# Optimization experiments

Measured on AMD Instinct MI355X. Metric: run time of the kernel, lower is better.

The kernel has to match this reference:

```python
import jax, jax.numpy as jnp
import numpy as np

# 5x5 neighborhood offsets as (dx, dy), row-major as in the original delta list
DELTA = [(dx, dy) for dy in (-2, -1, 0, 1, 2) for dx in (-2, -1, 0, 1, 2)]
BN_EPS = 1e-5


def _conv(x, w, padding):
    return jax.lax.conv_general_dilated(
        x, w, window_strides=(1, 1), padding=padding,
        dimension_numbers=('NCHW', 'OIHW', 'NCHW'))


def setup_inputs() -> dict:
    key = jax.random.key(0)
    ks = jax.random.split(key, 4)
    B, C, H, W = 128, 256, 24, 24
    source_feature = jax.random.normal(ks[0], (B, C, H, W), jnp.float32)
    detection_feature = jax.random.normal(ks[1], (B, C, H, W), jnp.float32)
    w1 = jax.random.normal(ks[2], (256, 512, 3, 3), jnp.float32) * 0.02
    b1 = jnp.zeros((256,), jnp.float32)
    bn_gamma = jnp.ones((256,), jnp.float32)
    bn_beta = jnp.zeros((256,), jnp.float32)
    bn_mean = jnp.zeros((256,), jnp.float32)
    bn_var = jnp.ones((256,), jnp.float32)
    w2 = jax.random.normal(ks[3], (25, 256, 1, 1), jnp.float32) * 0.05
    b2 = jnp.zeros((25,), jnp.float32)
    return dict(source_feature=source_feature, detection_feature=detection_feature,
                w1=w1, b1=b1, bn_gamma=bn_gamma, bn_beta=bn_beta,
                bn_mean=bn_mean, bn_var=bn_var, w2=w2, b2=b2)


def reference(source_feature, detection_feature, w1, b1, bn_gamma, bn_beta,
              bn_mean, bn_var, w2, b2):
    B, C, H, W = source_feature.shape
    # kernel_pre: Conv3x3(512->256, pad 1) + BN + ReLU + Conv1x1(256->25)
    concat_f = jnp.concatenate([source_feature, detection_feature], axis=1)  # [B,512,H,W]
    x = _conv(concat_f, w1, ((1, 1), (1, 1))) + b1[None, :, None, None]
    inv = bn_gamma / jnp.sqrt(bn_var + BN_EPS)
    x = x * inv[None, :, None, None] + (bn_beta - bn_mean * inv)[None, :, None, None]
    x = jax.nn.relu(x)
    logits = _conv(x, w2, ((0, 0), (0, 0))) + b2[None, :, None, None]  # [B,25,H,W]
    # per-pixel softmax over the 25 neighborhood taps
    kmaps = jax.nn.softmax(logits, axis=1)  # [B,25,H,W]
    # propagate: softmax-weighted 5x5 neighbor gather-sum; out-of-bounds taps
    # contribute zero (matches the skipped-boundary terms in the original loop)
    padded = jnp.pad(source_feature, ((0, 0), (0, 0), (2, 2), (2, 2)))
    prop = jnp.zeros_like(source_feature)
    for order, (dx, dy) in enumerate(DELTA):
        shifted = padded[:, :, 2 + dy:2 + dy + H, 2 + dx:2 + dx + W]  # [B,C,H,W]
        prop = prop + shifted * kmaps[:, order][:, None]  # broadcast over C
    return prop
```

## Files before the change

kernel.cpp:

```cpp
#include <hip/hip_runtime.h>
#include <hip/hip_bf16.h>
#include <stdint.h>

#define BATCH 128
#define CIN   256
#define CCAT  512
#define HH    24
#define WW    24
#define HP    26
#define WP    26
#define COUT  256
#define KDIM  4608
#define NPIX  576
#define MDIM  73728
#define NORD  25

typedef __attribute__((ext_vector_type(8))) short bf16x8;
typedef __attribute__((ext_vector_type(4))) float f32x4;

__device__ __forceinline__ unsigned short f2bf(float v) {
    union { float f; unsigned u; } x; x.f = v;
    unsigned r = x.u + 0x7fffu + ((x.u >> 16) & 1u);
    return (unsigned short)(r >> 16);
}
__device__ __forceinline__ float bf_lo(unsigned w) {
    union { unsigned u; float f; } x; x.u = w << 16; return x.f;
}
__device__ __forceinline__ float bf_hi(unsigned w) {
    union { unsigned u; float f; } x; x.u = w & 0xffff0000u; return x.f;
}

__device__ __forceinline__ void async_copy16(const void* gsrc, void* ldst) {
    __builtin_amdgcn_global_load_lds(
        (const __attribute__((address_space(1))) unsigned int*)gsrc,
        (__attribute__((address_space(3))) unsigned int*)ldst, 16, 0, 0);
}

#define PTILE 192
#define LSTR  72
__global__ __launch_bounds__(256) void prep_transpose(
        const float* __restrict__ src, const float* __restrict__ det,
        unsigned short* __restrict__ apad) {
    __shared__ unsigned short lds[PTILE * LSTR];
    int pt = blockIdx.x;
    int cg = blockIdx.y;
    int b  = blockIdx.z;
    int c0 = cg * 64;
    int p0 = pt * PTILE;
    const float* inp = (c0 < CIN)
        ? (src + ((long)b * CIN + c0) * NPIX)
        : (det + ((long)b * CIN + (c0 - CIN)) * NPIX);
    int tid = threadIdx.x;

    #pragma unroll
    for (int it = 0; it < 12; it++) {
        int l  = it * 256 + tid;
        int cq = l / PTILE;
        int px = l - cq * PTILE;
        const float* pb = inp + (long)cq * 4 * NPIX + p0 + px;
        unsigned short v0 = f2bf(pb[0 * NPIX]);
        unsigned short v1 = f2bf(pb[1 * NPIX]);
        unsigned short v2 = f2bf(pb[2 * NPIX]);
        unsigned short v3 = f2bf(pb[3 * NPIX]);
        uint2 w;
        w.x = (unsigned)v0 | ((unsigned)v1 << 16);
        w.y = (unsigned)v2 | ((unsigned)v3 << 16);
        *(uint2*)&lds[px * LSTR + cq * 4] = w;
    }
    __syncthreads();

    #pragma unroll
    for (int it = 0; it < 6; it++) {
        int l   = it * 256 + tid;
        int px  = l >> 3;
        int ch8 = l & 7;
        uint4 w = *(const uint4*)&lds[px * LSTR + ch8 * 8];
        int p  = p0 + px;
        int y  = p / WW, x = p - y * WW;
        long o = (((long)b * HP + (y + 1)) * WP + (x + 1)) * CCAT + c0 + ch8 * 8;
        *(uint4*)(apad + o) = w;
    }
}

__global__ __launch_bounds__(256) void zero_halo(unsigned short* __restrict__ apad) {
    int t = blockIdx.x * 256 + threadIdx.x;
    int ch8 = t & 63;
    int r   = t >> 6;
    int hp  = r % 100;
    int b   = r / 100;
    int y, x;
    if (hp < 26)      { y = 0;       x = hp; }
    else if (hp < 52) { y = 25;      x = hp - 26; }
    else if (hp < 76) { y = hp - 51; x = 0; }
    else              { y = hp - 75; x = 25; }
    long o = (((long)b * HP + y) * WP + x) * CCAT + ch8 * 8;
    *(uint4*)(apad + o) = (uint4){0u, 0u, 0u, 0u};
}

__global__ __launch_bounds__(256) void prep_w(
        const float* __restrict__ w1, const float* __restrict__ b1,
        const float* __restrict__ gam, const float* __restrict__ bet,
        const float* __restrict__ mu, const float* __restrict__ var,
        unsigned short* __restrict__ bt,
        float* __restrict__ scale, float* __restrict__ shift) {
    int idx = blockIdx.x * 256 + threadIdx.x;
    if (idx < COUT * KDIM) {
        int n = idx / KDIM;
        int k = idx - n * KDIM;
        int s = k >> 9;
        int ci = k & 511;
        int ky = s / 3, kx = s - ky * 3;
        float v = w1[(((long)n * 512 + ci) * 3 + ky) * 3 + kx];
        bt[idx] = f2bf(v);
    }
    if (blockIdx.x == 0 && threadIdx.x < COUT) {
        int c = threadIdx.x;
        float inv = gam[c] * rsqrtf(var[c] + 1e-5f);
        scale[c] = inv;
        shift[c] = (b1[c] - mu[c]) * inv + bet[c];
    }
}

#define STAGE_A(j, nb, soff) \
    async_copy16(apad + aSrc[j] + (soff), (void*)&lds[(nb)*32768 + (j)*4096 + w*512])
#define STAGE_B(j, nb, koff) \
    async_copy16(bt + bSrc[j] + (koff), (void*)&lds[(nb)*32768 + 16384 + (j)*4096 + w*512])
#define BAR()  __builtin_amdgcn_s_barrier()
#define WAITV2() { asm volatile("s_waitcnt vmcnt(2)" ::: "memory"); }
#define WAITV0() { asm volatile("s_waitcnt vmcnt(0)" ::: "memory"); }
#define WAITL()  { asm volatile("s_waitcnt lgkmcnt(0)" ::: "memory"); __builtin_amdgcn_sched_barrier(0); }

__global__ __launch_bounds__(512, 2) void conv1_gemm(
        const unsigned short* __restrict__ apad,
        const unsigned short* __restrict__ bt,
        const float* __restrict__ scale, const float* __restrict__ shift,
        unsigned short* __restrict__ xout) {
    __shared__ unsigned short lds[65536];
    const int tid  = threadIdx.x;
    const int w    = tid >> 6;
    const int lane = tid & 63;
    const int wr = w >> 2, wc = w & 3;
    const int fr = lane & 15, ls = lane >> 4;
    const long m0 = (long)blockIdx.x * 256;

    const int rowq = tid >> 3;
    const int sl   = (tid & 7) ^ (rowq & 7);
    long aSrc[4], bSrc[4];
    #pragma unroll
    for (int j = 0; j < 4; j++) {
        int r = j * 64 + rowq;
        long m = m0 + r;
        int b  = (int)(m / NPIX);
        int rr = (int)(m - (long)b * NPIX);
        int y = rr / WW, x = rr - y * WW;
        aSrc[j] = (((long)b * HP + y) * WP + x) * (long)CCAT + sl * 8;
        bSrc[j] = (long)r * KDIM + sl * 8;
    }

    const int rb   = fr & 7;
    const int csw0 = ((ls    ) ^ rb) << 4;
    const int csw1 = ((ls + 4) ^ rb) << 4;
    const int aBase = (wr * 128 + fr) * 128;
    const int bBase = 32768 + (wc * 64 + fr) * 128;

    f32x4 acc[8][4];
    #pragma unroll
    for (int i = 0; i < 8; i++)
        #pragma unroll
        for (int j = 0; j < 4; j++) acc[i][j] = (f32x4){0.f, 0.f, 0.f, 0.f};

    STAGE_B(0, 0, 0); STAGE_B(1, 0, 0); STAGE_B(2, 0, 0); STAGE_B(3, 0, 0);
    STAGE_A(0, 0, 0); STAGE_A(2, 0, 0); STAGE_A(1, 0, 0); STAGE_A(3, 0, 0);
    WAITV2();
    BAR();

    bf16x8 afr[4], bfr[4];
    int nb = 0;
    for (int kt = 0; kt < 71; kt++) {
        const int ktn = kt + 1;
        const int seg = ktn >> 3;
        const int ky = seg / 3, kx = seg - ky * 3;
        const long soff = (long)(ky * WP + kx) * CCAT + (ktn & 7) * 64;
        const long koff = (long)ktn * 64;
        const int pb = nb ^ 1;
        const char* L = (const char*)lds + nb * 65536;

        #pragma unroll
        for (int n = 0; n < 4; n++)
            bfr[n] = *(const bf16x8*)(L + bBase + n * 2048 + csw0);
        #pragma unroll
        for (int m = 0; m < 4; m++)
            afr[m] = *(const bf16x8*)(L + aBase + m * 2048 + csw0);
        STAGE_B(0, pb, koff); STAGE_B(1, pb, koff);
        WAITV2();
        BAR(); WAITL();
        __builtin_amdgcn_s_setprio(1);
        #pragma unroll
        for (int m = 0; m < 4; m++)
            #pragma unroll
            for (int n = 0; n < 4; n++)
                acc[m][n] = __builtin_amdgcn_mfma_f32_16x16x32_bf16(afr[m], bfr[n], acc[m][n], 0, 0, 0);
        __builtin_amdgcn_s_setprio(0);
        BAR();

        #pragma unroll
        for (int m = 0; m < 4; m++)
            afr[m] = *(const bf16x8*)(L + aBase + 8192 + m * 2048 + csw0);
        STAGE_B(2, pb, koff); STAGE_B(3, pb, koff);
        BAR(); WAITL();
        __builtin_amdgcn_s_setprio(1);
        #pragma unroll
        for (int m = 0; m < 4; m++)
            #pragma unroll
            for (int n = 0; n < 4; n++)
                acc[4 + m][n] = __builtin_amdgcn_mfma_f32_16x16x32_bf16(afr[m], bfr[n], acc[4 + m][n], 0, 0, 0);
        __builtin_amdgcn_s_setprio(0);
        BAR();

        #pragma unroll
        for (int n = 0; n < 4; n++)
            bfr[n] = *(const bf16x8*)(L + bBase + n * 2048 + csw1);
        #pragma unroll
        for (int m = 0; m < 4; m++)
            afr[m] = *(const bf16x8*)(L + aBase + m * 2048 + csw1);
        STAGE_A(0, pb, soff); STAGE_A(2, pb, soff);
        BAR(); WAITL();
        __builtin_amdgcn_s_setprio(1);
        #pragma unroll
        for (int m = 0; m < 4; m++)
            #pragma unroll
            for (int n = 0; n < 4; n++)
                acc[m][n] = __builtin_amdgcn_mfma_f32_16x16x32_bf16(afr[m], bfr[n], acc[m][n], 0, 0, 0);
        __builtin_amdgcn_s_setprio(0);
        BAR();

        #pragma unroll
        for (int m = 0; m < 4; m++)
            afr[m] = *(const bf16x8*)(L + aBase + 8192 + m * 2048 + csw1);
        STAGE_A(1, pb, soff); STAGE_A(3, pb, soff);
        WAITV2();
        BAR(); WAITL();
        __builtin_amdgcn_s_setprio(1);
        #pragma unroll
        for (int m = 0; m < 4; m++)
            #pragma unroll
            for (int n = 0; n < 4; n++)
                acc[4 + m][n] = __builtin_amdgcn_mfma_f32_16x16x32_bf16(afr[m], bfr[n], acc[4 + m][n], 0, 0, 0);
        __builtin_amdgcn_s_setprio(0);
        BAR();

        nb ^= 1;
    }

    {
        const char* L = (const char*)lds + nb * 65536;
        #pragma unroll
        for (int n = 0; n < 4; n++)
            bfr[n] = *(const bf16x8*)(L + bBase + n * 2048 + csw0);
        #pragma unroll
        for (int m = 0; m < 4; m++)
            afr[m] = *(const bf16x8*)(L + aBase + m * 2048 + csw0);
        WAITV0();
        BAR(); WAITL();
        #pragma unroll
        for (int m = 0; m < 4; m++)
            #pragma unroll
            for (int n = 0; n < 4; n++)
                acc[m][n] = __builtin_amdgcn_mfma_f32_16x16x32_bf16(afr[m], bfr[n], acc[m][n], 0, 0, 0);
        BAR();
        #pragma unroll
        for (int m = 0; m < 4; m++)
            afr[m] = *(const bf16x8*)(L + aBase + 8192 + m * 2048 + csw0);
        WAITL();
        #pragma unroll
        for (int m = 0; m < 4; m++)
            #pragma unroll
            for (int n = 0; n < 4; n++)
                acc[4 + m][n] = __builtin_amdgcn_mfma_f32_16x16x32_bf16(afr[m], bfr[n], acc[4 + m][n], 0, 0, 0);
        #pragma unroll
        for (int n = 0; n < 4; n++)
            bfr[n] = *(const bf16x8*)(L + bBase + n * 2048 + csw1);
        #pragma unroll
        for (int m = 0; m < 4; m++)
            afr[m] = *(const bf16x8*)(L + aBase + m * 2048 + csw1);
        WAITL();
        #pragma unroll
        for (int m = 0; m < 4; m++)
            #pragma unroll
            for (int n = 0; n < 4; n++)
                acc[m][n] = __builtin_amdgcn_mfma_f32_16x16x32_bf16(afr[m], bfr[n], acc[m][n], 0, 0, 0);
        #pragma unroll
        for (int m = 0; m < 4; m++)
            afr[m] = *(const bf16x8*)(L + aBase + 8192 + m * 2048 + csw1);
        WAITL();
        #pragma unroll
        for (int m = 0; m < 4; m++)
            #pragma unroll
            for (int n = 0; n < 4; n++)
                acc[4 + m][n] = __builtin_amdgcn_mfma_f32_16x16x32_bf16(afr[m], bfr[n], acc[4 + m][n], 0, 0, 0);
    }

    #pragma unroll
    for (int n = 0; n < 4; n++) {
        int col = wc * 64 + n * 16 + fr;
        float sc = scale[col], sh = shift[col];
        #pragma unroll
        for (int m = 0; m < 8; m++) {
            long rbase = m0 + wr * 128 + m * 16 + ls * 4;
            #pragma unroll
            for (int j = 0; j < 4; j++) {
                float v = acc[m][n][j] * sc + sh;
                v = v > 0.f ? v : 0.f;
                xout[(rbase + j) * COUT + col] = f2bf(v);
            }
        }
    }
}

__global__ __launch_bounds__(256) void conv2_softmax(
        const unsigned short* __restrict__ x, const float* __restrict__ w2,
        const float* __restrict__ b2, float* __restrict__ kmaps) {
    __shared__ float w2s[NORD * 256];
    __shared__ float b2s[NORD];
    for (int i = threadIdx.x; i < NORD * 256; i += 256) w2s[i] = w2[i];
    if (threadIdx.x < NORD) b2s[threadIdx.x] = b2[threadIdx.x];
    __syncthreads();
    long pix = (long)blockIdx.x * 256 + threadIdx.x;
    float acc[NORD];
    #pragma unroll
    for (int o = 0; o < NORD; o++) acc[o] = b2s[o];
    const unsigned short* xr = x + pix * COUT;
    for (int kc = 0; kc < 32; kc++) {
        uint4 raw = *(const uint4*)(xr + kc * 8);
        float xf[8];
        xf[0] = bf_lo(raw.x); xf[1] = bf_hi(raw.x);
        xf[2] = bf_lo(raw.y); xf[3] = bf_hi(raw.y);
        xf[4] = bf_lo(raw.z); xf[5] = bf_hi(raw.z);
        xf[6] = bf_lo(raw.w); xf[7] = bf_hi(raw.w);
        #pragma unroll
        for (int o = 0; o < NORD; o++) {
            const float* wrow = &w2s[o * 256 + kc * 8];
            float4 wa = *(const float4*)(wrow);
            float4 wb = *(const float4*)(wrow + 4);
            acc[o] += xf[0] * wa.x + xf[1] * wa.y + xf[2] * wa.z + xf[3] * wa.w
                    + xf[4] * wb.x + xf[5] * wb.y + xf[6] * wb.z + xf[7] * wb.w;
        }
    }
    float mx = acc[0];
    #pragma unroll
    for (int o = 1; o < NORD; o++) mx = fmaxf(mx, acc[o]);
    float s = 0.f;
    #pragma unroll
    for (int o = 0; o < NORD; o++) { acc[o] = expf(acc[o] - mx); s += acc[o]; }
    float inv = 1.f / s;
    float* kout = kmaps + pix * NORD;
    #pragma unroll
    for (int o = 0; o < NORD; o++) kout[o] = acc[o] * inv;
}

__global__ __launch_bounds__(576) void propagate(
        const float* __restrict__ src, const float* __restrict__ kmaps,
        float* __restrict__ out) {
    __shared__ float sm[28 * 28];
    int b  = blockIdx.y;
    int cg = blockIdx.x;
    int tid = threadIdx.x;
    int y = tid / 24, x = tid - y * 24;
    float km[NORD];
    const float* kp = kmaps + ((long)b * NPIX + tid) * NORD;
    #pragma unroll
    for (int o = 0; o < NORD; o++) km[o] = kp[o];
    for (int c = 0; c < 16; c++) {
        int cc = cg * 16 + c;
        const float* sp = src + ((long)b * CIN + cc) * NPIX;
        __syncthreads();
        for (int t = tid; t < 28 * 28; t += 576) {
            int yy = t / 28, xx = t - yy * 28;
            float v = 0.f;
            if (yy >= 2 && yy < 26 && xx >= 2 && xx < 26)
                v = sp[(yy - 2) * 24 + (xx - 2)];
            sm[t] = v;
        }
        __syncthreads();
        float a = 0.f;
        #pragma unroll
        for (int o = 0; o < NORD; o++) {
            int dy = o / 5 - 2, dx = o % 5 - 2;
            a += km[o] * sm[(y + 2 + dy) * 28 + (x + 2 + dx)];
        }
        out[((long)b * CIN + cc) * NPIX + tid] = a;
    }
}

extern "C" void kernel_launch(void* const* d_in, const int* in_sizes, int n_in,
                              void* d_out, int out_size, void* d_ws, size_t ws_size,
                              hipStream_t stream) {
    const float* src = (const float*)d_in[0];
    const float* det = (const float*)d_in[1];
    const float* w1  = (const float*)d_in[2];
    const float* b1  = (const float*)d_in[3];
    const float* gam = (const float*)d_in[4];
    const float* bet = (const float*)d_in[5];
    const float* mu  = (const float*)d_in[6];
    const float* var = (const float*)d_in[7];
    const float* w2  = (const float*)d_in[8];
    const float* b2  = (const float*)d_in[9];
    float* out = (float*)d_out;

    char* ws = (char*)d_ws;
    size_t off = 0;
    unsigned short* apad = (unsigned short*)(ws + off); off += (size_t)BATCH * HP * WP * CCAT * 2;
    unsigned short* bt   = (unsigned short*)(ws + off); off += (size_t)COUT * KDIM * 2;
    unsigned short* xbuf = (unsigned short*)(ws + off); off += (size_t)MDIM * COUT * 2;
    float* kmaps = (float*)(ws + off); off += (size_t)MDIM * NORD * 4;
    float* scale = (float*)(ws + off); off += 1024;
    float* shift = (float*)(ws + off); off += 1024;

    zero_halo<<<3200, 256, 0, stream>>>(apad);
    prep_transpose<<<dim3(3, 8, BATCH), 256, 0, stream>>>(src, det, apad);
    prep_w<<<4608, 256, 0, stream>>>(w1, b1, gam, bet, mu, var, bt, scale, shift);
    conv1_gemm<<<288, 512, 0, stream>>>(apad, bt, scale, shift, xbuf);
    conv2_softmax<<<288, 256, 0, stream>>>(xbuf, w2, b2, kmaps);
    propagate<<<dim3(16, BATCH), 576, 0, stream>>>(src, kmaps, out);
}
```

Before: 417.7 us.

## Shrink conv GEMM tile to 192x128 with grid remap and reordered staging

```diff
diff --git a/kernel.cpp b/kernel.cpp
--- a/kernel.cpp
+++ b/kernel.cpp
@@ -121,10 +121,12 @@
     }
 }
 
+#define ABUF_SH 12288
+#define BUF_SH  20480
 #define STAGE_A(j, nb, soff) \
-    async_copy16(apad + aSrc[j] + (soff), (void*)&lds[(nb)*32768 + (j)*4096 + w*512])
+    async_copy16(apad + aSrc[j] + (soff), (void*)&lds[(nb)*BUF_SH + (j)*4096 + w*512])
 #define STAGE_B(j, nb, koff) \
-    async_copy16(bt + bSrc[j] + (koff), (void*)&lds[(nb)*32768 + 16384 + (j)*4096 + w*512])
+    async_copy16(bt + bSrc[j] + (koff), (void*)&lds[(nb)*BUF_SH + ABUF_SH + (j)*4096 + w*512])
 #define BAR()  __builtin_amdgcn_s_barrier()
 #define WAITV2() { asm volatile("s_waitcnt vmcnt(2)" ::: "memory"); }
 #define WAITV0() { asm volatile("s_waitcnt vmcnt(0)" ::: "memory"); }
@@ -135,46 +137,50 @@
         const unsigned short* __restrict__ bt,
         const float* __restrict__ scale, const float* __restrict__ shift,
         unsigned short* __restrict__ xout) {
-    __shared__ unsigned short lds[65536];
+    __shared__ unsigned short lds[40960];
     const int tid  = threadIdx.x;
     const int w    = tid >> 6;
     const int lane = tid & 63;
     const int wr = w >> 2, wc = w & 3;
     const int fr = lane & 15, ls = lane >> 4;
-    const long m0 = (long)blockIdx.x * 256;
+
+    const int Lb = blockIdx.x;
+    const int logical = (Lb & 7) * 96 + (Lb >> 3);
+    const int n0 = (logical & 1) * 128;
+    const long m0 = (long)(logical >> 1) * 192;
 
     const int rowq = tid >> 3;
     const int sl   = (tid & 7) ^ (rowq & 7);
-    long aSrc[4], bSrc[4];
-    #pragma unroll
-    for (int j = 0; j < 4; j++) {
+    long aSrc[3], bSrc[2];
+    #pragma unroll
+    for (int j = 0; j < 3; j++) {
         int r = j * 64 + rowq;
         long m = m0 + r;
         int b  = (int)(m / NPIX);
         int rr = (int)(m - (long)b * NPIX);
         int y = rr / WW, x = rr - y * WW;
         aSrc[j] = (((long)b * HP + y) * WP + x) * (long)CCAT + sl * 8;
-        bSrc[j] = (long)r * KDIM + sl * 8;
-    }
+    }
+    #pragma unroll
+    for (int j = 0; j < 2; j++)
+        bSrc[j] = (long)(n0 + j * 64 + rowq) * KDIM + sl * 8;
 
     const int rb   = fr & 7;
     const int csw0 = ((ls    ) ^ rb) << 4;
     const int csw1 = ((ls + 4) ^ rb) << 4;
-    const int aBase = (wr * 128 + fr) * 128;
-    const int bBase = 32768 + (wc * 64 + fr) * 128;
-
-    f32x4 acc[8][4];
-    #pragma unroll
-    for (int i = 0; i < 8; i++)
-        #pragma unroll
-        for (int j = 0; j < 4; j++) acc[i][j] = (f32x4){0.f, 0.f, 0.f, 0.f};
-
-    STAGE_B(0, 0, 0); STAGE_B(1, 0, 0); STAGE_B(2, 0, 0); STAGE_B(3, 0, 0);
-    STAGE_A(0, 0, 0); STAGE_A(2, 0, 0); STAGE_A(1, 0, 0); STAGE_A(3, 0, 0);
-    WAITV2();
-    BAR();
-
-    bf16x8 afr[4], bfr[4];
+    const int aBase = (wr * 96 + fr) * 128;
+    const int bBase = 24576 + (wc * 32 + fr) * 128;
+
+    f32x4 acc[6][2];
+    #pragma unroll
+    for (int i = 0; i < 6; i++)
+        #pragma unroll
+        for (int j = 0; j < 2; j++) acc[i][j] = (f32x4){0.f, 0.f, 0.f, 0.f};
+
+    STAGE_B(0, 0, 0); STAGE_B(1, 0, 0);
+    STAGE_A(0, 0, 0); STAGE_A(1, 0, 0); STAGE_A(2, 0, 0);
+
+    bf16x8 afr[3], bfr[2];
     int nb = 0;
     for (int kt = 0; kt < 71; kt++) {
         const int ktn = kt + 1;
@@ -183,69 +189,67 @@
         const long soff = (long)(ky * WP + kx) * CCAT + (ktn & 7) * 64;
         const long koff = (long)ktn * 64;
         const int pb = nb ^ 1;
-        const char* L = (const char*)lds + nb * 65536;
-
-        #pragma unroll
-        for (int n = 0; n < 4; n++)
-            bfr[n] = *(const bf16x8*)(L + bBase + n * 2048 + csw0);
-        #pragma unroll
-        for (int m = 0; m < 4; m++)
-            afr[m] = *(const bf16x8*)(L + aBase + m * 2048 + csw0);
+        const char* L = (const char*)lds + nb * (BUF_SH * 2);
+
         STAGE_B(0, pb, koff); STAGE_B(1, pb, koff);
         WAITV2();
-        BAR(); WAITL();
+        BAR();
+        #pragma unroll
+        for (int n = 0; n < 2; n++)
+            bfr[n] = *(const bf16x8*)(L + bBase + n * 2048 + csw0);
+        #pragma unroll
+        for (int m = 0; m < 3; m++)
+            afr[m] = *(const bf16x8*)(L + aBase + m * 2048 + csw0);
+        WAITL();
         __builtin_amdgcn_s_setprio(1);
         #pragma unroll
-        for (int m = 0; m < 4; m++)
-            #pragma unroll
-            for (int n = 0; n < 4; n++)
+        for (int m = 0; m < 3; m++)
+            #pragma unroll
+            for (int n = 0; n < 2; n++)
                 acc[m][n] = __builtin_amdgcn_mfma_f32_16x16x32_bf16(afr[m], bfr[n], acc[m][n], 0, 0, 0);
         __builtin_amdgcn_s_setprio(0);
         BAR();
 
         #pragma unroll
-        for (int m = 0; m < 4; m++)
-            afr[m] = *(const bf16x8*)(L + aBase + 8192 + m * 2048 + csw0);
-        STAGE_B(2, pb, koff); STAGE_B(3, pb, koff);
-        BAR(); WAITL();
+        for (int m = 0; m < 3; m++)
+            afr[m] = *(const bf16x8*)(L + aBase + (3 + m) * 2048 + csw0);
+        STAGE_A(0, pb, soff); STAGE_A(1, pb, soff); STAGE_A(2, pb, soff);
+        WAITL();
         __builtin_amdgcn_s_setprio(1);
         #pragma unroll
-        for (int m = 0; m < 4; m++)
-            #pragma unroll
-            for (int n = 0; n < 4; n++)
-                acc[4 + m][n] = __builtin_amdgcn_mfma_f32_16x16x32_bf16(afr[m], bfr[n], acc[4 + m][n], 0, 0, 0);
+        for (int m = 0; m < 3; m++)
+            #pragma unroll
+            for (int n = 0; n < 2; n++)
+                acc[3 + m][n] = __builtin_amdgcn_mfma_f32_16x16x32_bf16(afr[m], bfr[n], acc[3 + m][n], 0, 0, 0);
         __builtin_amdgcn_s_setprio(0);
         BAR();
 
         #pragma unroll
-        for (int n = 0; n < 4; n++)
+        for (int n = 0; n < 2; n++)
             bfr[n] = *(const bf16x8*)(L + bBase + n * 2048 + csw1);
         #pragma unroll
-        for (int m = 0; m < 4; m++)
+        for (int m = 0; m < 3; m++)
             afr[m] = *(const bf16x8*)(L + aBase + m * 2048 + csw1);
-        STAGE_A(0, pb, soff); STAGE_A(2, pb, soff);
-        BAR(); WAITL();
+        WAITL();
         __builtin_amdgcn_s_setprio(1);
         #pragma unroll
-        for (int m = 0; m < 4; m++)
-            #pragma unroll
-            for (int n = 0; n < 4; n++)
+        for (int m = 0; m < 3; m++)
+            #pragma unroll
+            for (int n = 0; n < 2; n++)
                 acc[m][n] = __builtin_amdgcn_mfma_f32_16x16x32_bf16(afr[m], bfr[n], acc[m][n], 0, 0, 0);
         __builtin_amdgcn_s_setprio(0);
         BAR();
 
         #pragma unroll
-        for (int m = 0; m < 4; m++)
-            afr[m] = *(const bf16x8*)(L + aBase + 8192 + m * 2048 + csw1);
-        STAGE_A(1, pb, soff); STAGE_A(3, pb, soff);
-        WAITV2();
-        BAR(); WAITL();
+        for (int m = 0; m < 3; m++)
+            afr[m] = *(const bf16x8*)(L + aBase + (3 + m) * 2048 + csw1);
+        WAITL();
         __builtin_amdgcn_s_setprio(1);
         #pragma unroll
-        for (int m = 0; m < 4; m++)
-            #pragma unroll
-            for (int n = 0; n < 4; n++)
-                acc[4 + m][n] = __builtin_amdgcn_mfma_f32_16x16x32_bf16(afr[m], bfr[n], acc[4 + m][n], 0, 0, 0);
+        for (int m = 0; m < 3; m++)
+            #pragma unroll
+            for (int n = 0; n < 2; n++)
+                acc[3 + m][n] = __builtin_amdgcn_mfma_f32_16x16x32_bf16(afr[m], bfr[n], acc[3 + m][n], 0, 0, 0);
         __builtin_amdgcn_s_setprio(0);
         BAR();
 
@@ -253,60 +257,60 @@
     }
 
     {
-        const char* L = (const char*)lds + nb * 65536;
-        #pragma unroll
-        for (int n = 0; n < 4; n++)
+        const char* L = (const char*)lds + nb * (BUF_SH * 2);
+        WAITV0();
+        BAR();
+        #pragma unroll
+        for (int n = 0; n < 2; n++)
             bfr[n] = *(const bf16x8*)(L + bBase + n * 2048 + csw0);
         #pragma unroll
-        for (int m = 0; m < 4; m++)
+        for (int m = 0; m < 3; m++)
             afr[m] = *(const bf16x8*)(L + aBase + m * 2048 + csw0);
-        WAITV0();
-        BAR(); WAITL();
-        #pragma unroll
-        for (int m = 0; m < 4; m++)
-            #pragma unroll
-            for (int n = 0; n < 4; n++)
+        WAITL();
+        #pragma unroll
+        for (int m = 0; m < 3; m++)
+            #pragma unroll
+            for (int n = 0; n < 2; n++)
                 acc[m][n] = __builtin_amdgcn_mfma_f32_16x16x32_bf16(afr[m], bfr[n], acc[m][n], 0, 0, 0);
-        BAR();
-        #pragma unroll
-        for (int m = 0; m < 4; m++)
-            afr[m] = *(const bf16x8*)(L + aBase + 8192 + m * 2048 + csw0);
-        WAITL();
-        #pragma unroll
-        for (int m = 0; m < 4; m++)
-            #pragma unroll
-            for (int n = 0; n < 4; n++)
-                acc[4 + m][n] = __builtin_amdgcn_mfma_f32_16x16x32_bf16(afr[m], bfr[n], acc[4 + m][n], 0, 0, 0);
-        #pragma unroll
-        for (int n = 0; n < 4; n++)
+        #pragma unroll
+        for (int m = 0; m < 3; m++)
+            afr[m] = *(const bf16x8*)(L + aBase + (3 + m) * 2048 + csw0);
+        WAITL();
+        #pragma unroll
+        for (int m = 0; m < 3; m++)
+            #pragma unroll
+            for (int n = 0; n < 2; n++)
+                acc[3 + m][n] = __builtin_amdgcn_mfma_f32_16x16x32_bf16(afr[m], bfr[n], acc[3 + m][n], 0, 0, 0);
+        #pragma unroll
+        for (int n = 0; n < 2; n++)
             bfr[n] = *(const bf16x8*)(L + bBase + n * 2048 + csw1);
         #pragma unroll
-        for (int m = 0; m < 4; m++)
+        for (int m = 0; m < 3; m++)
             afr[m] = *(const bf16x8*)(L + aBase + m * 2048 + csw1);
         WAITL();
         #pragma unroll
-        for (int m = 0; m < 4; m++)
-            #pragma unroll
-            for (int n = 0; n < 4; n++)
+        for (int m = 0; m < 3; m++)
+            #pragma unroll
+            for (int n = 0; n < 2; n++)
                 acc[m][n] = __builtin_amdgcn_mfma_f32_16x16x32_bf16(afr[m], bfr[n], acc[m][n], 0, 0, 0);
         #pragma unroll
-        for (int m = 0; m < 4; m++)
-            afr[m] = *(const bf16x8*)(L + aBase + 8192 + m * 2048 + csw1);
-        WAITL();
-        #pragma unroll
-        for (int m = 0; m < 4; m++)
-            #pragma unroll
-            for (int n = 0; n < 4; n++)
-                acc[4 + m][n] = __builtin_amdgcn_mfma_f32_16x16x32_bf16(afr[m], bfr[n], acc[4 + m][n], 0, 0, 0);
-    }
-
-    #pragma unroll
-    for (int n = 0; n < 4; n++) {
-        int col = wc * 64 + n * 16 + fr;
+        for (int m = 0; m < 3; m++)
+            afr[m] = *(const bf16x8*)(L + aBase + (3 + m) * 2048 + csw1);
+        WAITL();
+        #pragma unroll
+        for (int m = 0; m < 3; m++)
+            #pragma unroll
+            for (int n = 0; n < 2; n++)
+                acc[3 + m][n] = __builtin_amdgcn_mfma_f32_16x16x32_bf16(afr[m], bfr[n], acc[3 + m][n], 0, 0, 0);
+    }
+
+    #pragma unroll
+    for (int n = 0; n < 2; n++) {
+        int col = n0 + wc * 32 + n * 16 + fr;
         float sc = scale[col], sh = shift[col];
         #pragma unroll
-        for (int m = 0; m < 8; m++) {
-            long rbase = m0 + wr * 128 + m * 16 + ls * 4;
+        for (int m = 0; m < 6; m++) {
+            long rbase = m0 + wr * 96 + m * 16 + ls * 4;
             #pragma unroll
             for (int j = 0; j < 4; j++) {
                 float v = acc[m][n][j] * sc + sh;
@@ -419,7 +423,7 @@
     zero_halo<<<3200, 256, 0, stream>>>(apad);
     prep_transpose<<<dim3(3, 8, BATCH), 256, 0, stream>>>(src, det, apad);
     prep_w<<<4608, 256, 0, stream>>>(w1, b1, gam, bet, mu, var, bt, scale, shift);
-    conv1_gemm<<<288, 512, 0, stream>>>(apad, bt, scale, shift, xbuf);
+    conv1_gemm<<<768, 512, 0, stream>>>(apad, bt, scale, shift, xbuf);
     conv2_softmax<<<288, 256, 0, stream>>>(xbuf, w2, b2, kmaps);
     propagate<<<dim3(16, BATCH), 576, 0, stream>>>(src, kmaps, out);
 }
```

Result: faster. 358.7 us (-14.1%).
